# Kernel tuning notes

Measured on AMD Instinct MI355X. Metric: run time of the kernel, lower is better.

The kernel has to match this reference:

```python
import jax, jax.numpy as jnp
import numpy as np

EPS = 1e-5

def setup_inputs() -> dict:
    key = jax.random.key(0)
    k1, k2, k3 = jax.random.split(key, 3)
    B, D, H = 8192, 1536, 16384
    x = jax.random.normal(k1, (B, D), dtype=jnp.float32)
    # torch Linear default init ~ U(-1/sqrt(fan_in), 1/sqrt(fan_in)); scaled normal is fine for a reference
    W_enc = jax.random.normal(k2, (H, D), dtype=jnp.float32) * (1.0 / np.sqrt(D))
    W_dec = jax.random.normal(k3, (D, H), dtype=jnp.float32) * (1.0 / np.sqrt(H))
    pre_bias = jnp.zeros((D,), dtype=jnp.float32)
    latent_bias = jnp.zeros((H,), dtype=jnp.float32)
    return {"x": x, "W_enc": W_enc, "W_dec": W_dec,
            "pre_bias": pre_bias, "latent_bias": latent_bias, "k": 64}


def reference(x, W_enc, W_dec, pre_bias, latent_bias, k):
    # ---- LN preprocess (torch .std uses Bessel correction, ddof=1) ----
    mu = jnp.mean(x, axis=-1, keepdims=True)          # [B,1]
    xc = x - mu
    std = jnp.std(xc, axis=-1, keepdims=True, ddof=1)  # [B,1]
    xn = xc / (std + EPS)

    # ---- encode: Linear(bias=False) on (xn - pre_bias), add latent_bias ----
    h = jnp.einsum('bd,hd->bh', xn - pre_bias, W_enc) + latent_bias  # [B,H]
    h = jax.nn.relu(h)

    # ---- topk sparsity: keep values >= k-th largest per row ----
    topk_vals = jax.lax.top_k(h, k)[0]                # [B,k]
    threshold = topk_vals[:, -1:]                     # [B,1]
    h_sparse = h * (h >= threshold)

    # ---- decode + denormalize ----
    recon = jnp.einsum('bh,dh->bd', h_sparse, W_dec) + pre_bias
    recon = recon * std + mu

    # ---- metrics (as arrays instead of .item()) ----
    sparsity_ratio = jnp.mean(jnp.mean((h_sparse == 0).astype(jnp.float32), axis=1))
    abs_h = jnp.abs(h_sparse)
    mean_activation = jnp.mean(abs_h)
    std_activation = jnp.std(abs_h, ddof=1)
    return recon, h_sparse, sparsity_ratio, mean_activation, std_activation
```

## Files before the change

kernel.cpp:

```cpp
#include <hip/hip_runtime.h>
#include <hip/hip_bf16.h>
#include <math.h>

static constexpr int Bn = 8192;
static constexpr int Hn = 16384;
static constexpr int Dn = 1536;
static constexpr int KTOP = 64;
static constexpr int KE = 1536;
static constexpr int WSTR = 2048;
static constexpr double EPSD = 1e-5;

static constexpr size_t MU_OFF  = 0;
static constexpr size_t STD_OFF = 32768;
static constexpr size_t CNT_OFF = 98304;
static constexpr size_t NNZ_OFF = 131072;
static constexpr size_t SUM_OFF = 131200;
static constexpr size_t MUD_OFF = 262144;
static constexpr size_t RID_OFF = 327680;
static constexpr size_t IDX_OFF = (size_t)1 << 20;
static constexpr size_t VAL_OFF = (size_t)6 << 20;
static constexpr size_t AP_OFF  = (size_t)16 << 20;
static constexpr size_t BP_OFF  = (size_t)48 << 20;
static constexpr size_t WT_OFF  = (size_t)104 << 20;
static constexpr size_t H16_OFF = (size_t)176 << 20;

typedef __attribute__((ext_vector_type(8))) short short8;
typedef __attribute__((ext_vector_type(4))) float f32x4;

static __device__ __forceinline__ unsigned short f2bf(float f) {
    __hip_bfloat16 b = __float2bfloat16(f);
    return *reinterpret_cast<unsigned short*>(&b);
}
static __device__ __forceinline__ float bf2f(unsigned short u) {
    return __uint_as_float(((unsigned)u) << 16);
}
static __device__ __forceinline__ void gload_lds16(const void* g, void* l) {
    __builtin_amdgcn_global_load_lds(
        (const __attribute__((address_space(1))) unsigned int*)g,
        (__attribute__((address_space(3))) unsigned int*)l, 16, 0, 0);
}

__global__ void k_zero(unsigned* nnz, double* sums) {
    if (threadIdx.x == 0) { *nnz = 0u; sums[0] = 0.0; sums[1] = 0.0; }
}

__global__ __launch_bounds__(256) void k_rowstats(const float* __restrict__ x,
                                                  const float* __restrict__ pre_bias,
                                                  double* __restrict__ muD,
                                                  double* __restrict__ rinvD,
                                                  float* __restrict__ muF,
                                                  float* __restrict__ stdF,
                                                  unsigned short* __restrict__ Ap) {
    const int row = blockIdx.x;
    const int tid = threadIdx.x;
    const float* xr = x + (size_t)row * Dn;
    float v[6];
#pragma unroll
    for (int i = 0; i < 6; ++i) v[i] = xr[tid + 256 * i];
    double s = 0.0;
#pragma unroll
    for (int i = 0; i < 6; ++i) s += (double)v[i];
    __shared__ double redD[4];
    __shared__ double smu, srin;
#pragma unroll
    for (int o = 32; o > 0; o >>= 1) s += __shfl_down(s, o);
    if ((tid & 63) == 0) redD[tid >> 6] = s;
    __syncthreads();
    if (tid == 0) smu = (redD[0] + redD[1] + redD[2] + redD[3]) / (double)Dn;
    __syncthreads();
    const double m = smu;
    double q = 0.0;
#pragma unroll
    for (int i = 0; i < 6; ++i) { double d = (double)v[i] - m; q += d * d; }
#pragma unroll
    for (int o = 32; o > 0; o >>= 1) q += __shfl_down(q, o);
    if ((tid & 63) == 0) redD[tid >> 6] = q;
    __syncthreads();
    if (tid == 0) {
        double var = (redD[0] + redD[1] + redD[2] + redD[3]) / (double)(Dn - 1);
        double sd = sqrt(var);
        muD[row] = m;
        srin = 1.0 / (sd + EPSD);
        rinvD[row] = srin;
        muF[row] = (float)m;
        stdF[row] = (float)sd;
    }
    __syncthreads();
    const double ri = srin;
    unsigned short* ar = Ap + (size_t)row * KE;
#pragma unroll
    for (int i = 0; i < 6; ++i) {
        const int d = tid + i * 256;
        double a = ((double)v[i] - m) * ri - (double)pre_bias[d];
        ar[d] = f2bf((float)a);
    }
}

__global__ __launch_bounds__(256) void k_splitW(const float* __restrict__ Wenc,
                                                unsigned short* __restrict__ Bp) {
    const int row = blockIdx.x;
    const int tid = threadIdx.x;
    const float2* wr = (const float2*)(Wenc + (size_t)row * Dn);
    ushort2* br = (ushort2*)(Bp + (size_t)row * KE);
#pragma unroll
    for (int i = 0; i < 3; ++i) {
        float2 w = wr[tid + i * 256];
        ushort2 o; o.x = f2bf(w.x); o.y = f2bf(w.y);
        br[tid + i * 256] = o;
    }
}

__global__ __launch_bounds__(256) void k_transpose(const float* __restrict__ Wdec,
                                                   unsigned short* __restrict__ WdecT) {
    __shared__ float tile[32][33];
    const int h0 = blockIdx.x * 32;
    const int d0 = blockIdx.y * 32;
    const int tx = threadIdx.x & 31;
    const int ty = threadIdx.x >> 5;
#pragma unroll
    for (int r = 0; r < 4; ++r) {
        int d = ty + r * 8;
        tile[d][tx] = Wdec[(size_t)(d0 + d) * Hn + h0 + tx];
    }
    __syncthreads();
#pragma unroll
    for (int r = 0; r < 4; ++r) {
        int h = ty + r * 8;
        WdecT[(size_t)(h0 + h) * WSTR + d0 + tx] = f2bf(tile[tx][h]);
    }
}

__global__ __launch_bounds__(512, 2) void k_gemm(const unsigned short* __restrict__ Ap,
                                                 const unsigned short* __restrict__ Bp,
                                                 const float* __restrict__ lat_bias,
                                                 unsigned short* __restrict__ hout16) {
    __shared__ unsigned short AsBuf[2][256 * 64];
    __shared__ unsigned short BsBuf[2][256 * 64];
    const int tid = threadIdx.x;
    const int lane = tid & 63;
    const int w = tid >> 6;
    const int wm = w >> 2;
    const int wn = w & 3;

    const int nwg = (Bn / 256) * (Hn / 256);
    int swz = (blockIdx.x % 8) * (nwg / 8) + blockIdx.x / 8;
    int st = swz >> 6;
    int wi = swz & 63;
    int stm = st >> 3, stn = st & 7;
    const int bm = stm * 8 + (wi >> 3);
    const int bn = stn * 8 + (wi & 7);

    const size_t arow0 = (size_t)(bm * 256) * KE;
    const size_t brow0 = (size_t)(bn * 256) * KE;

    #define STAGE_TILE(kt, buf)                                                   \
        {                                                                         \
            _Pragma("unroll")                                                     \
            for (int l = 0; l < 4; ++l) {                                         \
                const int idx = l * 512 + tid;                                    \
                const int row = idx >> 3, slot = idx & 7;                         \
                const int ssl = slot ^ (row & 7);                                 \
                gload_lds16(Ap + arow0 + (size_t)row * KE + (kt) * 64 + ssl * 8,  \
                            (char*)AsBuf[buf] + idx * 16);                        \
                gload_lds16(Bp + brow0 + (size_t)row * KE + (kt) * 64 + ssl * 8,  \
                            (char*)BsBuf[buf] + idx * 16);                        \
            }                                                                     \
        }

    f32x4 acc[8][4];
#pragma unroll
    for (int i = 0; i < 8; ++i)
#pragma unroll
        for (int j = 0; j < 4; ++j) acc[i][j] = (f32x4){0.f, 0.f, 0.f, 0.f};

    constexpr int NT = KE / 64;
    STAGE_TILE(0, 0);
    STAGE_TILE(1, 1);
    asm volatile("s_waitcnt vmcnt(8)" ::: "memory");
    __builtin_amdgcn_s_barrier();
    asm volatile("" ::: "memory");

    for (int t = 0; t < NT; ++t) {
        const int buf = t & 1;
        const unsigned short* Ab = AsBuf[buf];
        const unsigned short* Bb = BsBuf[buf];
        short8 bfr[4][2];
#pragma unroll
        for (int fj = 0; fj < 4; ++fj)
#pragma unroll
            for (int kk = 0; kk < 2; ++kk) {
                const int br = wn * 64 + fj * 16 + (lane & 15);
                const int slot = (kk * 4 + (lane >> 4)) ^ (br & 7);
                bfr[fj][kk] = *(const short8*)((const char*)Bb + br * 128 + slot * 16);
            }
#pragma unroll
        for (int qm = 0; qm < 2; ++qm) {
            short8 afr[4][2];
#pragma unroll
            for (int fi = 0; fi < 4; ++fi)
#pragma unroll
                for (int kk = 0; kk < 2; ++kk) {
                    const int ar = wm * 128 + qm * 64 + fi * 16 + (lane & 15);
                    const int slot = (kk * 4 + (lane >> 4)) ^ (ar & 7);
                    afr[fi][kk] = *(const short8*)((const char*)Ab + ar * 128 + slot * 16);
                }
#pragma unroll
            for (int kk = 0; kk < 2; ++kk)
#pragma unroll
                for (int fi = 0; fi < 4; ++fi)
#pragma unroll
                    for (int fj = 0; fj < 4; ++fj)
                        acc[qm * 4 + fi][fj] = __builtin_amdgcn_mfma_f32_16x16x32_bf16(
                            afr[fi][kk], bfr[fj][kk], acc[qm * 4 + fi][fj], 0, 0, 0);
        }
        __builtin_amdgcn_s_barrier();
        asm volatile("" ::: "memory");
        if (t + 2 < NT) {
            STAGE_TILE(t + 2, buf);
            asm volatile("s_waitcnt vmcnt(8)" ::: "memory");
        } else {
            asm volatile("s_waitcnt vmcnt(0)" ::: "memory");
        }
        __builtin_amdgcn_s_barrier();
        asm volatile("" ::: "memory");
    }
    #undef STAGE_TILE

    const int col = lane & 15;
#pragma unroll
    for (int fj = 0; fj < 4; ++fj) {
        const int gn = bn * 256 + wn * 64 + fj * 16 + col;
        const float bias = lat_bias[gn];
#pragma unroll
        for (int fi8 = 0; fi8 < 8; ++fi8) {
            const int gm0 = bm * 256 + wm * 128 + fi8 * 16 + (lane >> 4) * 4;
#pragma unroll
            for (int r = 0; r < 4; ++r) {
                float vv = acc[fi8][fj][r] + bias;
                hout16[(size_t)(gm0 + r) * Hn + gn] = f2bf(fmaxf(vv, 0.f));
            }
        }
    }
}

__global__ __launch_bounds__(256) void k_topsel(const unsigned short* __restrict__ h16,
                                                const float* __restrict__ x,
                                                const float* __restrict__ Wenc,
                                                const float* __restrict__ pre_bias,
                                                const float* __restrict__ lat_bias,
                                                const double* __restrict__ muD,
                                                const double* __restrict__ rinvD,
                                                unsigned* __restrict__ counts,
                                                int* __restrict__ idx_list,
                                                float* __restrict__ val_list) {
    const int row = blockIdx.x;
    const int tid = threadIdx.x;
    const int lane = tid & 63;
    const int wid = tid >> 6;

    __shared__ unsigned short hrow[Hn];
    const unsigned short* hr16 = h16 + (size_t)row * Hn;
#pragma unroll
    for (int i = 0; i < 8; ++i)
        gload_lds16((const char*)hr16 + (i * 256 + tid) * 16,
                    (char*)hrow + (i * 256 + tid) * 16);
    __syncthreads();
    const unsigned* hl = (const unsigned*)hrow;

    __shared__ int wsum[4];
    __shared__ unsigned sbc;
    unsigned lo = 0, hi = 0xFFFFu;
    while (lo < hi) {
        const unsigned mid = (lo + hi + 1) >> 1;
        int c = 0;
#pragma unroll
        for (int j = 0; j < 32; ++j) {
            const unsigned uu = hl[j * 256 + tid];
            c += ((uu & 0xFFFFu) >= mid) ? 1 : 0;
            c += ((uu >> 16) >= mid) ? 1 : 0;
        }
#pragma unroll
        for (int o = 32; o > 0; o >>= 1) c += __shfl_down(c, o);
        if ((tid & 63) == 0) wsum[tid >> 6] = c;
        __syncthreads();
        if (tid == 0) sbc = (unsigned)(wsum[0] + wsum[1] + wsum[2] + wsum[3]);
        __syncthreads();
        if (sbc >= (unsigned)KTOP) lo = mid; else hi = mid - 1;
    }
    const float thr = bf2f((unsigned short)lo);
    const float DELTA = 0.02f;
    const float hi_t = thr + DELTA;
    const float lo_t = thr - DELTA;

    constexpr int MAXC = 128;
    __shared__ int s_g, s_c;
    __shared__ int cidx[MAXC];
    __shared__ double cvalD[MAXC];
    __shared__ float cref[MAXC];
    __shared__ unsigned char csel[MAXC];
    __shared__ unsigned long long kmask[256];
    __shared__ unsigned ccnt[256];
    __shared__ unsigned cinc[256];
    if (tid == 0) { s_g = 0; s_c = 0; }
    __syncthreads();
    int g_loc = 0;
#pragma unroll
    for (int j = 0; j < 32; ++j) {
        const unsigned uu = hl[j * 256 + tid];
        float v0 = bf2f((unsigned short)(uu & 0xFFFFu));
        float v1 = bf2f((unsigned short)(uu >> 16));
        const int i0 = 2 * (j * 256 + tid);
        if (v0 > hi_t) g_loc++;
        else if (v0 >= lo_t) {
            int p = atomicAdd(&s_c, 1);
            if (p < MAXC) cidx[p] = i0;
        }
        if (v1 > hi_t) g_loc++;
        else if (v1 >= lo_t) {
            int p = atomicAdd(&s_c, 1);
            if (p < MAXC) cidx[p] = i0 + 1;
        }
    }
    if (g_loc) atomicAdd(&s_g, g_loc);
    __syncthreads();
    const int ec = (s_c < MAXC) ? s_c : MAXC;

    {
        const double rmu = muD[row];
        const double rin = rinvD[row];
        const float* xr = x + (size_t)row * Dn;
        for (int e = wid; e < ec; e += 4) {
            const int feat = cidx[e];
            const float* wr = Wenc + (size_t)feat * Dn;
            double acc = 0.0;
            for (int d = lane; d < Dn; d += 64) {
                double xn = ((double)xr[d] - rmu) * rin - (double)pre_bias[d];
                acc = fma(xn, (double)wr[d], acc);
            }
#pragma unroll
            for (int o = 32; o > 0; o >>= 1) acc += __shfl_down(acc, o);
            if (lane == 0) {
                double hv = acc + (double)lat_bias[feat];
                cvalD[e] = hv;
                float hf = (float)hv;
                cref[e] = hf > 0.f ? hf : 0.f;
            }
        }
    }
    __syncthreads();
    if (tid == 0) {
        const int need = KTOP - s_g;
        for (int e = 0; e < ec; ++e) csel[e] = 0;
        for (int it = 0; it < need && it < ec; ++it) {
            int best = -1; double bv = -1e300; int bidx = 1 << 30;
            for (int e = 0; e < ec; ++e) {
                if (csel[e]) continue;
                if (cvalD[e] > bv || (cvalD[e] == bv && cidx[e] < bidx)) {
                    bv = cvalD[e]; best = e; bidx = cidx[e];
                }
            }
            if (best >= 0) csel[best] = 1;
        }
    }
    __syncthreads();

    for (int i = 0; i < 64; ++i) {
        const int c = wid * 64 + i;
        const int f = c * 64 + lane;
        const float val = bf2f(hrow[f]);
        bool keep;
        if (val > hi_t) keep = true;
        else if (val >= lo_t) {
            keep = false;
            for (int e = 0; e < ec; ++e)
                if (cidx[e] == f) { keep = (csel[e] != 0); break; }
        } else keep = false;
        unsigned long long bm = __ballot(keep);
        if (lane == 0) { kmask[c] = bm; ccnt[c] = (unsigned)__popcll(bm); }
    }
    __syncthreads();
    cinc[tid] = ccnt[tid];
    __syncthreads();
#pragma unroll
    for (int o = 1; o < 256; o <<= 1) {
        unsigned t = cinc[tid] + ((tid >= o) ? cinc[tid - o] : 0u);
        __syncthreads();
        cinc[tid] = t;
        __syncthreads();
    }
    if (tid == 0) {
        unsigned tot = cinc[255];
        counts[row] = tot < 128u ? tot : 128u;
    }
    __syncthreads();
    for (int i = 0; i < 64; ++i) {
        const int c = wid * 64 + i;
        const unsigned long long bm = kmask[c];
        if (!bm) continue;
        if ((bm >> lane) & 1ull) {
            unsigned pos = (cinc[c] - ccnt[c]) +
                           (unsigned)__popcll(bm & ((1ull << lane) - 1ull));
            if (pos < 128u) {
                const int f = c * 64 + lane;
                float sv = bf2f(hrow[f]);
                if (sv >= lo_t && sv <= hi_t) {
                    for (int e = 0; e < ec; ++e)
                        if (cidx[e] == f) { sv = cref[e]; break; }
                }
                idx_list[(size_t)row * 128 + pos] = f;
                val_list[(size_t)row * 128 + pos] = sv;
            }
        }
    }
}

__global__ __launch_bounds__(256) void k_hwdec(const unsigned* __restrict__ counts,
                                               const int* __restrict__ idx_list,
                                               const float* __restrict__ val_list,
                                               const unsigned short* __restrict__ WdecT,
                                               const float* __restrict__ pre_bias,
                                               const float* __restrict__ muF,
                                               const float* __restrict__ stdF,
                                               float* __restrict__ outh,
                                               float* __restrict__ outr,
                                               unsigned* __restrict__ nnz_acc,
                                               double* __restrict__ sums) {
    const int row = blockIdx.x;
    const int tid = threadIdx.x;
    const unsigned cnt = counts[row];
    __shared__ int sidx[128];
    __shared__ float sval[128];
    if (tid < (int)cnt) {
        sidx[tid] = idx_list[(size_t)row * 128 + tid];
        sval[tid] = val_list[(size_t)row * 128 + tid];
    }
    float* orow = outh + (size_t)row * Hn;
    float4* orow16 = (float4*)orow;
    const float4 z = {0.f, 0.f, 0.f, 0.f};
#pragma unroll
    for (int i = 0; i < 16; ++i) orow16[tid + i * 256] = z;
    __syncthreads();
    float val = 0.f;
    if (tid < (int)cnt) { orow[sidx[tid]] = sval[tid]; val = sval[tid]; }
    float s1 = val, s2 = val * val;
    __shared__ float r1[4], r2[4];
#pragma unroll
    for (int o = 32; o > 0; o >>= 1) {
        s1 += __shfl_down(s1, o);
        s2 += __shfl_down(s2, o);
    }
    if ((tid & 63) == 0) { r1[tid >> 6] = s1; r2[tid >> 6] = s2; }
    __syncthreads();
    if (tid == 0) {
        atomicAdd(sums + 0, (double)(r1[0] + r1[1] + r1[2] + r1[3]));
        atomicAdd(sums + 1, (double)(r2[0] + r2[1] + r2[2] + r2[3]));
        atomicAdd(nnz_acc, cnt);
    }
    if (tid >= 192) return;
    float a[8] = {0.f, 0.f, 0.f, 0.f, 0.f, 0.f, 0.f, 0.f};
    float b[8] = {0.f, 0.f, 0.f, 0.f, 0.f, 0.f, 0.f, 0.f};
    const size_t toff = (size_t)tid * 8;
    unsigned j = 0;
    for (; j + 2 <= cnt; j += 2) {
        short8 w0 = *(const short8*)(WdecT + (size_t)sidx[j] * WSTR + toff);
        short8 w1 = *(const short8*)(WdecT + (size_t)sidx[j + 1] * WSTR + toff);
        const float v0 = sval[j], v1 = sval[j + 1];
#pragma unroll
        for (int i = 0; i < 8; ++i) {
            a[i] = fmaf(v0, bf2f((unsigned short)w0[i]), a[i]);
            b[i] = fmaf(v1, bf2f((unsigned short)w1[i]), b[i]);
        }
    }
    if (j < cnt) {
        short8 w0 = *(const short8*)(WdecT + (size_t)sidx[j] * WSTR + toff);
        const float v0 = sval[j];
#pragma unroll
        for (int i = 0; i < 8; ++i)
            a[i] = fmaf(v0, bf2f((unsigned short)w0[i]), a[i]);
    }
    const float m_ = muF[row], s_ = stdF[row];
    const int d0 = tid * 8;
    float o[8];
#pragma unroll
    for (int i = 0; i < 8; ++i)
        o[i] = ((a[i] + b[i]) + pre_bias[d0 + i]) * s_ + m_;
    float* rrow = outr + (size_t)row * Dn + d0;
    *(float4*)(rrow)     = *(float4*)&o[0];
    *(float4*)(rrow + 4) = *(float4*)&o[4];
}

__global__ void k_final(const unsigned* __restrict__ nnz,
                        const double* __restrict__ sums,
                        float* __restrict__ out3) {
    if (threadIdx.x == 0) {
        const double N = (double)Bn * (double)Hn;
        const double nz = (double)(*nnz);
        const double sparsity = (N - nz) / N;
        const double mean = sums[0] / N;
        double var = (sums[1] - N * mean * mean) / (N - 1.0);
        if (var < 0.0) var = 0.0;
        out3[0] = (float)sparsity;
        out3[1] = (float)mean;
        out3[2] = (float)sqrt(var);
    }
}

extern "C" void kernel_launch(void* const* d_in, const int* in_sizes, int n_in,
                              void* d_out, int out_size, void* d_ws, size_t ws_size,
                              hipStream_t stream) {
    const float* x        = (const float*)d_in[0];
    const float* Wenc     = (const float*)d_in[1];
    const float* Wdec     = (const float*)d_in[2];
    const float* pre_bias = (const float*)d_in[3];
    const float* lat_bias = (const float*)d_in[4];

    char* ws = (char*)d_ws;
    float*          muF    = (float*)(ws + MU_OFF);
    float*          stdF   = (float*)(ws + STD_OFF);
    unsigned*       counts = (unsigned*)(ws + CNT_OFF);
    unsigned*       nnz    = (unsigned*)(ws + NNZ_OFF);
    double*         sums   = (double*)(ws + SUM_OFF);
    double*         muD    = (double*)(ws + MUD_OFF);
    double*         rinvD  = (double*)(ws + RID_OFF);
    int*            idxl   = (int*)(ws + IDX_OFF);
    float*          vall   = (float*)(ws + VAL_OFF);
    unsigned short* Ap     = (unsigned short*)(ws + AP_OFF);
    unsigned short* Bp     = (unsigned short*)(ws + BP_OFF);
    unsigned short* WdecT  = (unsigned short*)(ws + WT_OFF);
    unsigned short* h16    = (unsigned short*)(ws + H16_OFF);

    float* out       = (float*)d_out;
    float* out_recon = out;
    float* out_h     = out + (size_t)Bn * Dn;
    float* out_sc    = out + (size_t)Bn * Dn + (size_t)Bn * Hn;

    hipLaunchKernelGGL(k_zero, dim3(1), dim3(64), 0, stream, nnz, sums);
    hipLaunchKernelGGL(k_rowstats, dim3(Bn), dim3(256), 0, stream,
                       x, pre_bias, muD, rinvD, muF, stdF, Ap);
    hipLaunchKernelGGL(k_splitW, dim3(Hn), dim3(256), 0, stream, Wenc, Bp);
    hipLaunchKernelGGL(k_transpose, dim3(Hn / 32, Dn / 32), dim3(256), 0, stream, Wdec, WdecT);
    hipLaunchKernelGGL(k_gemm, dim3((Bn / 256) * (Hn / 256)), dim3(512), 0, stream,
                       Ap, Bp, lat_bias, h16);
    hipLaunchKernelGGL(k_topsel, dim3(Bn), dim3(256), 0, stream,
                       h16, x, Wenc, pre_bias, lat_bias, muD, rinvD,
                       counts, idxl, vall);
    hipLaunchKernelGGL(k_hwdec, dim3(Bn), dim3(256), 0, stream,
                       counts, idxl, vall, WdecT, pre_bias, muF, stdF,
                       out_h, out_recon, nnz, sums);
    hipLaunchKernelGGL(k_final, dim3(1), dim3(64), 0, stream, nnz, sums, out_sc);
}
```

Baseline: 1.586 ms.

## Replace bisection threshold search with two-pass radix histogram select in top-k

The per-row top-k threshold search changes from a 16-step binary search over the whole row to a two-level 8-bit radix histogram built with shared-memory atomics and suffix scans. The row is no longer staged in LDS; global memory is read directly several times. The compaction now uses wave-level shuffle scans and per-lane masks instead of a block-wide scan over shared arrays. This cuts passes and barriers, but adds atomic contention and repeated global reads, and zero-valued keys are excluded from the histogram.

```diff
diff --git a/kernel.cpp b/kernel.cpp
--- a/kernel.cpp
+++ b/kernel.cpp
@@ -257,37 +257,65 @@
     const int tid = threadIdx.x;
     const int lane = tid & 63;
     const int wid = tid >> 6;
-
-    __shared__ unsigned short hrow[Hn];
     const unsigned short* hr16 = h16 + (size_t)row * Hn;
-#pragma unroll
-    for (int i = 0; i < 8; ++i)
-        gload_lds16((const char*)hr16 + (i * 256 + tid) * 16,
-                    (char*)hrow + (i * 256 + tid) * 16);
-    __syncthreads();
-    const unsigned* hl = (const unsigned*)hrow;
-
-    __shared__ int wsum[4];
-    __shared__ unsigned sbc;
-    unsigned lo = 0, hi = 0xFFFFu;
-    while (lo < hi) {
-        const unsigned mid = (lo + hi + 1) >> 1;
-        int c = 0;
-#pragma unroll
-        for (int j = 0; j < 32; ++j) {
-            const unsigned uu = hl[j * 256 + tid];
-            c += ((uu & 0xFFFFu) >= mid) ? 1 : 0;
-            c += ((uu >> 16) >= mid) ? 1 : 0;
-        }
-#pragma unroll
-        for (int o = 32; o > 0; o >>= 1) c += __shfl_down(c, o);
-        if ((tid & 63) == 0) wsum[tid >> 6] = c;
+    const unsigned* hu = (const unsigned*)hr16;
+
+    __shared__ unsigned hist[4][256];
+    __shared__ unsigned sfx[256];
+    __shared__ int sSel, sRem;
+
+#pragma unroll
+    for (int b = 0; b < 4; ++b) hist[b][tid] = 0;
+    if (tid == 0) { sSel = 0; sRem = KTOP; }
+    __syncthreads();
+#pragma unroll
+    for (int j = 0; j < 32; ++j) {
+        const unsigned uu = hu[j * 256 + tid];
+        const unsigned k0 = uu & 0xFFFFu, k1 = uu >> 16;
+        if (k0) atomicAdd(&hist[wid][k0 >> 8], 1u);
+        if (k1) atomicAdd(&hist[wid][k1 >> 8], 1u);
+    }
+    __syncthreads();
+    sfx[tid] = hist[0][tid] + hist[1][tid] + hist[2][tid] + hist[3][tid];
+    __syncthreads();
+#pragma unroll
+    for (int o = 1; o < 256; o <<= 1) {
+        unsigned t = sfx[tid] + ((tid + o < 256) ? sfx[tid + o] : 0u);
         __syncthreads();
-        if (tid == 0) sbc = (unsigned)(wsum[0] + wsum[1] + wsum[2] + wsum[3]);
+        sfx[tid] = t;
         __syncthreads();
-        if (sbc >= (unsigned)KTOP) lo = mid; else hi = mid - 1;
-    }
-    const float thr = bf2f((unsigned short)lo);
+    }
+    if (sfx[tid] >= (unsigned)KTOP && (tid == 255 || sfx[tid + 1] < (unsigned)KTOP)) {
+        sSel = tid;
+        sRem = KTOP - (tid == 255 ? 0 : (int)sfx[tid + 1]);
+    }
+    __syncthreads();
+    const unsigned hbSel = (unsigned)sSel;
+    const int remain = sRem;
+#pragma unroll
+    for (int b = 0; b < 4; ++b) hist[b][tid] = 0;
+    __syncthreads();
+#pragma unroll
+    for (int j = 0; j < 32; ++j) {
+        const unsigned uu = hu[j * 256 + tid];
+        const unsigned k0 = uu & 0xFFFFu, k1 = uu >> 16;
+        if (k0 && (k0 >> 8) == hbSel) atomicAdd(&hist[wid][k0 & 255u], 1u);
+        if (k1 && (k1 >> 8) == hbSel) atomicAdd(&hist[wid][k1 & 255u], 1u);
+    }
+    __syncthreads();
+    sfx[tid] = hist[0][tid] + hist[1][tid] + hist[2][tid] + hist[3][tid];
+    __syncthreads();
+#pragma unroll
+    for (int o = 1; o < 256; o <<= 1) {
+        unsigned t = sfx[tid] + ((tid + o < 256) ? sfx[tid + o] : 0u);
+        __syncthreads();
+        sfx[tid] = t;
+        __syncthreads();
+    }
+    if (sfx[tid] >= (unsigned)remain && (tid == 255 || sfx[tid + 1] < (unsigned)remain))
+        sSel = (int)((hbSel << 8) | (unsigned)tid);
+    __syncthreads();
+    const float thr = bf2f((unsigned short)sSel);
     const float DELTA = 0.02f;
     const float hi_t = thr + DELTA;
     const float lo_t = thr - DELTA;
@@ -298,15 +326,12 @@
     __shared__ double cvalD[MAXC];
     __shared__ float cref[MAXC];
     __shared__ unsigned char csel[MAXC];
-    __shared__ unsigned long long kmask[256];
-    __shared__ unsigned ccnt[256];
-    __shared__ unsigned cinc[256];
     if (tid == 0) { s_g = 0; s_c = 0; }
     __syncthreads();
     int g_loc = 0;
 #pragma unroll
     for (int j = 0; j < 32; ++j) {
-        const unsigned uu = hl[j * 256 + tid];
+        const unsigned uu = hu[j * 256 + tid];
         float v0 = bf2f((unsigned short)(uu & 0xFFFFu));
         float v1 = bf2f((unsigned short)(uu >> 16));
         const int i0 = 2 * (j * 256 + tid);
@@ -364,10 +389,11 @@
     }
     __syncthreads();
 
+    unsigned long long mymask = 0ull;
+    int mycnt = 0;
     for (int i = 0; i < 64; ++i) {
-        const int c = wid * 64 + i;
-        const int f = c * 64 + lane;
-        const float val = bf2f(hrow[f]);
+        const int f = (wid * 64 + i) * 64 + lane;
+        const float val = bf2f(hr16[f]);
         bool keep;
         if (val > hi_t) keep = true;
         else if (val >= lo_t) {
@@ -376,33 +402,36 @@
                 if (cidx[e] == f) { keep = (csel[e] != 0); break; }
         } else keep = false;
         unsigned long long bm = __ballot(keep);
-        if (lane == 0) { kmask[c] = bm; ccnt[c] = (unsigned)__popcll(bm); }
-    }
-    __syncthreads();
-    cinc[tid] = ccnt[tid];
-    __syncthreads();
-#pragma unroll
-    for (int o = 1; o < 256; o <<= 1) {
-        unsigned t = cinc[tid] + ((tid >= o) ? cinc[tid - o] : 0u);
-        __syncthreads();
-        cinc[tid] = t;
-        __syncthreads();
-    }
-    if (tid == 0) {
-        unsigned tot = cinc[255];
-        counts[row] = tot < 128u ? tot : 128u;
-    }
-    __syncthreads();
+        if (lane == i) { mymask = bm; mycnt = (int)__popcll(bm); }
+    }
+    int p = mycnt;
+#pragma unroll
+    for (int o = 1; o < 64; o <<= 1) {
+        int u = __shfl_up(p, o);
+        if (lane >= o) p += u;
+    }
+    __shared__ int wtot[4];
+    if (lane == 63) wtot[wid] = p;
+    __syncthreads();
+    int wbase = 0, total = 0;
+#pragma unroll
+    for (int ww = 0; ww < 4; ++ww) {
+        if (ww < wid) wbase += wtot[ww];
+        total += wtot[ww];
+    }
+    if (tid == 0) counts[row] = (unsigned)(total < 128 ? total : 128);
+
     for (int i = 0; i < 64; ++i) {
-        const int c = wid * 64 + i;
-        const unsigned long long bm = kmask[c];
+        const unsigned long long bm = __shfl(mymask, i);
         if (!bm) continue;
+        const int cnt_i = __shfl(mycnt, i);
+        const int pfx_i = __shfl(p, i);
         if ((bm >> lane) & 1ull) {
-            unsigned pos = (cinc[c] - ccnt[c]) +
-                           (unsigned)__popcll(bm & ((1ull << lane) - 1ull));
-            if (pos < 128u) {
-                const int f = c * 64 + lane;
-                float sv = bf2f(hrow[f]);
+            int pos = wbase + (pfx_i - cnt_i) +
+                      (int)__popcll(bm & ((1ull << lane) - 1ull));
+            if (pos < 128) {
+                const int f = (wid * 64 + i) * 64 + lane;
+                float sv = bf2f(hr16[f]);
                 if (sv >= lo_t && sv <= hi_t) {
                     for (int e = 0; e < ec; ++e)
                         if (cidx[e] == f) { sv = cref[e]; break; }
```

Result: slower. 1.846 ms (+16.4%).
